# Performance work log

Hardware: AMD Instinct MI355X
Metric: run time of the kernel (lower is better)

The kernel has to match this reference:

```python
import jax, jax.numpy as jnp
import numpy as np

EMBED_DIM = 1024
NUM_HEADS = 16
HEAD_DIM = EMBED_DIM // NUM_HEADS


def setup_inputs() -> dict:
    key = jax.random.key(0)
    ks = jax.random.split(key, 9)
    B, L, D = 4, 2048, EMBED_DIM
    s = 1.0 / np.sqrt(D)
    return {
        "inputs": jax.random.normal(ks[0], (B, L, D), dtype=jnp.float32),
        "wq": jax.random.normal(ks[1], (D, D), dtype=jnp.float32) * s,
        "bq": jax.random.normal(ks[2], (D,), dtype=jnp.float32) * s,
        "wk": jax.random.normal(ks[3], (D, D), dtype=jnp.float32) * s,
        "bk": jax.random.normal(ks[4], (D,), dtype=jnp.float32) * s,
        "wv": jax.random.normal(ks[5], (D, D), dtype=jnp.float32) * s,
        "bv": jax.random.normal(ks[6], (D,), dtype=jnp.float32) * s,
        "wo": jax.random.normal(ks[7], (D, D), dtype=jnp.float32) * s,
        "bo": jax.random.normal(ks[8], (D,), dtype=jnp.float32) * s,
    }


def reference(inputs, wq, bq, wk, bk, wv, bv, wo, bo):
    B, L, D = inputs.shape
    H, Hd = NUM_HEADS, HEAD_DIM
    # Linear projections (torch Linear: x @ W^T + b)
    q = inputs @ wq.T + bq
    k = inputs @ wk.T + bk
    v = inputs @ wv.T + bv
    # (B, L, D) -> (B, H, L, Hd)
    q = q.reshape(B, L, H, Hd).transpose(0, 2, 1, 3)
    k = k.reshape(B, L, H, Hd).transpose(0, 2, 1, 3)
    v = v.reshape(B, L, H, Hd).transpose(0, 2, 1, 3)
    scale = 1.0 / np.sqrt(Hd).astype(np.float32)
    scores = jnp.einsum("bhqd,bhkd->bhqk", q, k) * scale  # (B,H,L,L)
    attn = jax.nn.softmax(scores, axis=-1)
    out = jnp.einsum("bhqk,bhkd->bhqd", attn, v)  # (B,H,L,Hd)
    out = out.transpose(0, 2, 1, 3).reshape(B, L, D)
    return out @ wo.T + bo
```

## Files before the change

kernel.cpp:

```cpp
#include <hip/hip_runtime.h>

typedef __attribute__((ext_vector_type(8))) short short8;
typedef __attribute__((ext_vector_type(8))) unsigned short ushort8;
typedef __attribute__((ext_vector_type(4))) unsigned short ushort4_t;
typedef __attribute__((ext_vector_type(4))) unsigned u32x4;
typedef __attribute__((ext_vector_type(4))) float f32x4;
typedef __attribute__((ext_vector_type(16))) float f32x16;

#define GLOAD_LDS(gp, lp) \
  __builtin_amdgcn_global_load_lds((const __attribute__((address_space(1))) void*)(gp), \
                                   (__attribute__((address_space(3))) void*)(lp), 16, 0, 0)

static __device__ __forceinline__ unsigned short f2bf(float f) {
  unsigned int u = __float_as_uint(f);
  u = u + 0x7fffu + ((u >> 16) & 1u);
  return (unsigned short)(u >> 16);
}

static __device__ __forceinline__ float exp2i(float x) {
  float r;
  asm("v_exp_f32 %0, %1" : "=v"(r) : "v"(x));
  return r;
}

static __device__ __forceinline__ unsigned cvtpk(float a, float b) {
  unsigned r;
  asm("v_cvt_pk_bf16_f32 %0, %1, %2" : "=v"(r) : "v"(a), "v"(b));
  return r;
}

static __device__ __forceinline__ void pl32swap(unsigned& a, unsigned& b) {
  asm("v_permlane32_swap_b32 %0, %1" : "+v"(a), "+v"(b));
}

__global__ __launch_bounds__(256) void cvt_all(const float* __restrict__ X,
                                               const float* __restrict__ w0, const float* __restrict__ w1,
                                               const float* __restrict__ w2, const float* __restrict__ w3,
                                               unsigned short* __restrict__ Xb,
                                               unsigned short* __restrict__ o0, unsigned short* __restrict__ o1,
                                               unsigned short* __restrict__ o2, unsigned short* __restrict__ o3) {
  int bid = blockIdx.x;
  const float* in;
  unsigned short* out;
  int i;
  if (bid < 4096) {
    in = X; out = Xb; i = bid * 2048 + threadIdx.x * 8;
  } else {
    int idx = bid - 4096;
    int w = idx >> 9;
    in = (w == 0) ? w0 : (w == 1) ? w1 : (w == 2) ? w2 : w3;
    out = (w == 0) ? o0 : (w == 1) ? o1 : (w == 2) ? o2 : o3;
    i = (idx & 511) * 2048 + threadIdx.x * 8;
  }
  const float4* p = reinterpret_cast<const float4*>(in + i);
  float4 a = p[0], b = p[1];
  ushort8 o;
  o[0] = f2bf(a.x); o[1] = f2bf(a.y); o[2] = f2bf(a.z); o[3] = f2bf(a.w);
  o[4] = f2bf(b.x); o[5] = f2bf(b.y); o[6] = f2bf(b.z); o[7] = f2bf(b.w);
  *reinterpret_cast<ushort8*>(out + i) = o;
}

template <int MODE, int BN>
__global__ __launch_bounds__(256) void gemm_bt(const unsigned short* __restrict__ A,
                                               const unsigned short* __restrict__ B,
                                               const float* __restrict__ bias,
                                               void* __restrict__ Cptr,
                                               int M, int N, int K, float scale) {
  constexpr int BCH = BN / 32;
  constexpr int NI = BN / 32;
  __shared__ char As[2][16384];
  __shared__ char Bs[2][BN * 128];
  const int t = threadIdx.x;
  const int lane = t & 63, wave = t >> 6;
  const int wm = wave >> 1, wn = wave & 1;
  const int m0 = blockIdx.y * 128, n0 = blockIdx.x * BN;

  const unsigned short* aS[4];
  const unsigned short* bS[BCH];
#pragma unroll
  for (int j = 0; j < 4; j++) {
    int i = wave * 256 + j * 64 + lane;
    int r = i >> 3, c = ((i & 7) ^ (r & 7)) << 3;
    aS[j] = A + (size_t)(m0 + r) * K + c;
  }
#pragma unroll
  for (int j = 0; j < BCH; j++) {
    int i = wave * (64 * BCH) + j * 64 + lane;
    int r = i >> 3, c = ((i & 7) ^ (r & 7)) << 3;
    bS[j] = B + (size_t)(n0 + r) * K + c;
  }

  f32x4 acc[4][NI] = {};
  const int NT = K >> 6;

#pragma unroll
  for (int j = 0; j < 4; j++) GLOAD_LDS(aS[j], As[0] + wave * 4096 + j * 1024);
#pragma unroll
  for (int j = 0; j < BCH; j++) GLOAD_LDS(bS[j], Bs[0] + wave * (1024 * BCH) + j * 1024);

  for (int kt = 0; kt < NT; kt++) {
    const int cur = kt & 1;
    __syncthreads();
    if (kt + 1 < NT) {
      int ko = (kt + 1) << 6;
#pragma unroll
      for (int j = 0; j < 4; j++) GLOAD_LDS(aS[j] + ko, As[cur ^ 1] + wave * 4096 + j * 1024);
#pragma unroll
      for (int j = 0; j < BCH; j++) GLOAD_LDS(bS[j] + ko, Bs[cur ^ 1] + wave * (1024 * BCH) + j * 1024);
    }
    const char* Ac = As[cur];
    const char* Bc = Bs[cur];
#pragma unroll
    for (int ks = 0; ks < 2; ks++) {
      short8 af[4], bfr[NI];
#pragma unroll
      for (int x = 0; x < 4; x++) {
        int arow = wm * 64 + x * 16 + (lane & 15);
        int kk = ks * 32 + (lane >> 4) * 8;
        af[x] = *reinterpret_cast<const short8*>(Ac + (((arow * 64 + kk) * 2) ^ ((arow & 7) << 4)));
      }
#pragma unroll
      for (int x = 0; x < NI; x++) {
        int brow = wn * (BN / 2) + x * 16 + (lane & 15);
        int kk = ks * 32 + (lane >> 4) * 8;
        bfr[x] = *reinterpret_cast<const short8*>(Bc + (((brow * 64 + kk) * 2) ^ ((brow & 7) << 4)));
      }
      __builtin_amdgcn_s_setprio(1);
#pragma unroll
      for (int mi = 0; mi < 4; mi++)
#pragma unroll
        for (int ni = 0; ni < NI; ni++)
          acc[mi][ni] = __builtin_amdgcn_mfma_f32_16x16x32_bf16(af[mi], bfr[ni], acc[mi][ni], 0, 0, 0);
      __builtin_amdgcn_s_setprio(0);
    }
  }

#pragma unroll
  for (int mi = 0; mi < 4; mi++) {
#pragma unroll
    for (int ni = 0; ni < NI; ni++) {
      int n = n0 + wn * (BN / 2) + ni * 16 + (lane & 15);
      float bs = bias[n];
      int mbase = m0 + wm * 64 + mi * 16 + ((lane >> 4) << 2);
      if (MODE == 2) {
        int b = mbase >> 11, l = mbase & 2047;
        ushort4_t o;
#pragma unroll
        for (int r = 0; r < 4; r++) o[r] = f2bf(acc[mi][ni][r] + bs);
        *reinterpret_cast<ushort4_t*>((unsigned short*)Cptr + (size_t)(b * N + n) * 2048 + l) = o;
      } else if (MODE == 0) {
#pragma unroll
        for (int r = 0; r < 4; r++)
          ((unsigned short*)Cptr)[(size_t)(mbase + r) * N + n] = f2bf((acc[mi][ni][r] + bs) * scale);
      } else {
#pragma unroll
        for (int r = 0; r < 4; r++)
          ((float*)Cptr)[(size_t)(mbase + r) * N + n] = acc[mi][ni][r] + bs;
      }
    }
  }
}

__global__ __launch_bounds__(256, 4) void attn_fwd(const unsigned short* __restrict__ Q,
                                                   const unsigned short* __restrict__ Kb,
                                                   const unsigned short* __restrict__ Vt,
                                                   unsigned short* __restrict__ O) {
  const int orig = blockIdx.x;
  const int wgid = (orig & 7) * 128 + (orig >> 3);
  const int qt = wgid & 15;
  const int h = (wgid >> 4) & 15;
  const int b = wgid >> 8;
  const int q0 = qt * 128;

  __shared__ char Ks[2][8192];
  __shared__ char Vs[2][8192];
  const int t = threadIdx.x, lane = t & 63, wave = t >> 6;
  const int ql = lane & 31;
  const int hi = lane >> 5;
  const int qrow = q0 + wave * 32 + ql;
  const int sw = (ql & 7) << 4;

  int lo_[4];
#pragma unroll
  for (int st = 0; st < 4; st++) lo_[st] = (ql * 128 + sw) ^ (st * 32 + hi * 16);

  const int ic0 = wave * 128 + lane, ic1 = ic0 + 64;
  const int r0 = ic0 >> 3, c0 = ((ic0 & 7) ^ (r0 & 7)) << 3;
  const int r1 = ic1 >> 3, c1 = ((ic1 & 7) ^ (r1 & 7)) << 3;
  const unsigned short* kS0 = Kb + (size_t)(b * 2048 + r0) * 1024 + h * 64 + c0;
  const unsigned short* kS1 = Kb + (size_t)(b * 2048 + r1) * 1024 + h * 64 + c1;
  const unsigned short* vS0 = Vt + ((size_t)(b * 16 + h) * 64 + r0) * 2048 + c0;
  const unsigned short* vS1 = Vt + ((size_t)(b * 16 + h) * 64 + r1) * 2048 + c1;

  short8 qf[4];
  {
    const unsigned short* qp = Q + (size_t)(b * 2048 + qrow) * 1024 + h * 64 + hi * 8;
#pragma unroll
    for (int st = 0; st < 4; st++) qf[st] = *reinterpret_cast<const short8*>(qp + st * 16);
  }

  const short one_bf = (short)0x3F80;
  const short8 ones = {one_bf, one_bf, one_bf, one_bf, one_bf, one_bf, one_bf, one_bf};

  f32x16 accd0 = {}, accd1 = {};
  f32x16 accl = {};

  GLOAD_LDS(kS0, Ks[0] + wave * 2048);
  GLOAD_LDS(kS1, Ks[0] + wave * 2048 + 1024);
  GLOAD_LDS(vS0, Vs[0] + wave * 2048);
  GLOAD_LDS(vS1, Vs[0] + wave * 2048 + 1024);

#pragma unroll 2
  for (int kt = 0; kt < 32; kt++) {
    const int cur = kt & 1;
    __syncthreads();
    if (kt + 1 < 32) {
      size_t ko = (size_t)(kt + 1) * 65536;
      int vo = (kt + 1) * 64;
      GLOAD_LDS(kS0 + ko, Ks[cur ^ 1] + wave * 2048);
      GLOAD_LDS(kS1 + ko, Ks[cur ^ 1] + wave * 2048 + 1024);
      GLOAD_LDS(vS0 + vo, Vs[cur ^ 1] + wave * 2048);
      GLOAD_LDS(vS1 + vo, Vs[cur ^ 1] + wave * 2048 + 1024);
    }
    const char* Kc = Ks[cur];
    const char* Vc = Vs[cur];

    f32x16 s0 = {}, s1 = {};
    __builtin_amdgcn_s_setprio(1);
#pragma unroll
    for (int st = 0; st < 4; st++) {
      short8 k0 = *reinterpret_cast<const short8*>(Kc + lo_[st]);
      short8 k1 = *reinterpret_cast<const short8*>(Kc + lo_[st] + 4096);
      s0 = __builtin_amdgcn_mfma_f32_32x32x16_bf16(k0, qf[st], s0, 0, 0, 0);
      s1 = __builtin_amdgcn_mfma_f32_32x32x16_bf16(k1, qf[st], s1, 0, 0, 0);
    }
    __builtin_amdgcn_s_setprio(0);

    short8 pf0, pf1, pf2, pf3;
    {
#pragma unroll
      for (int r = 0; r < 16; r++) s0[r] = exp2i(s0[r]);
      unsigned w0 = cvtpk(s0[0], s0[1]), w1 = cvtpk(s0[2], s0[3]);
      unsigned w2 = cvtpk(s0[4], s0[5]), w3 = cvtpk(s0[6], s0[7]);
      pl32swap(w0, w2); pl32swap(w1, w3);
      u32x4 p0 = {w0, w1, w2, w3};
      pf0 = __builtin_bit_cast(short8, p0);
      unsigned w4 = cvtpk(s0[8], s0[9]), w5 = cvtpk(s0[10], s0[11]);
      unsigned w6 = cvtpk(s0[12], s0[13]), w7 = cvtpk(s0[14], s0[15]);
      pl32swap(w4, w6); pl32swap(w5, w7);
      u32x4 p1 = {w4, w5, w6, w7};
      pf1 = __builtin_bit_cast(short8, p1);
    }
    {
#pragma unroll
      for (int r = 0; r < 16; r++) s1[r] = exp2i(s1[r]);
      unsigned x0 = cvtpk(s1[0], s1[1]), x1 = cvtpk(s1[2], s1[3]);
      unsigned x2 = cvtpk(s1[4], s1[5]), x3 = cvtpk(s1[6], s1[7]);
      pl32swap(x0, x2); pl32swap(x1, x3);
      u32x4 p2 = {x0, x1, x2, x3};
      pf2 = __builtin_bit_cast(short8, p2);
      unsigned x4 = cvtpk(s1[8], s1[9]), x5 = cvtpk(s1[10], s1[11]);
      unsigned x6 = cvtpk(s1[12], s1[13]), x7 = cvtpk(s1[14], s1[15]);
      pl32swap(x4, x6); pl32swap(x5, x7);
      u32x4 p3 = {x4, x5, x6, x7};
      pf3 = __builtin_bit_cast(short8, p3);
    }

    __builtin_amdgcn_s_setprio(1);
#pragma unroll
    for (int st = 0; st < 4; st++) {
      short8 pb = (st == 0) ? pf0 : (st == 1) ? pf1 : (st == 2) ? pf2 : pf3;
      short8 v0 = *reinterpret_cast<const short8*>(Vc + lo_[st]);
      short8 v1 = *reinterpret_cast<const short8*>(Vc + lo_[st] + 4096);
      accd0 = __builtin_amdgcn_mfma_f32_32x32x16_bf16(v0, pb, accd0, 0, 0, 0);
      accd1 = __builtin_amdgcn_mfma_f32_32x32x16_bf16(v1, pb, accd1, 0, 0, 0);
      accl  = __builtin_amdgcn_mfma_f32_32x32x16_bf16(ones, pb, accl, 0, 0, 0);
    }
    __builtin_amdgcn_s_setprio(0);
  }

  float inv = 1.0f / accl[0];
  unsigned short* op = O + (size_t)(b * 2048 + qrow) * 1024 + h * 64;
#pragma unroll
  for (int g = 0; g < 4; g++) {
    ushort4_t o0, o1;
#pragma unroll
    for (int j = 0; j < 4; j++) {
      o0[j] = f2bf(accd0[4 * g + j] * inv);
      o1[j] = f2bf(accd1[4 * g + j] * inv);
    }
    *reinterpret_cast<ushort4_t*>(op + 8 * g + 4 * hi) = o0;
    *reinterpret_cast<ushort4_t*>(op + 32 + 8 * g + 4 * hi) = o1;
  }
}

extern "C" void kernel_launch(void* const* d_in, const int* in_sizes, int n_in,
                              void* d_out, int out_size, void* d_ws, size_t ws_size,
                              hipStream_t stream) {
  const float* X = (const float*)d_in[0];
  const float* wq = (const float*)d_in[1];
  const float* bq = (const float*)d_in[2];
  const float* wk = (const float*)d_in[3];
  const float* bk = (const float*)d_in[4];
  const float* wv = (const float*)d_in[5];
  const float* bv = (const float*)d_in[6];
  const float* wo = (const float*)d_in[7];
  const float* bo = (const float*)d_in[8];

  char* ws = (char*)d_ws;
  const size_t MB = 1024 * 1024;
  unsigned short* Xb  = (unsigned short*)(ws + 0);
  unsigned short* Wqb = (unsigned short*)(ws + 16 * MB);
  unsigned short* Wkb = (unsigned short*)(ws + 18 * MB);
  unsigned short* Wvb = (unsigned short*)(ws + 20 * MB);
  unsigned short* Wob = (unsigned short*)(ws + 22 * MB);
  unsigned short* Qb  = (unsigned short*)(ws + 24 * MB);
  unsigned short* Kb  = (unsigned short*)(ws + 40 * MB);
  unsigned short* Vtb = (unsigned short*)(ws + 56 * MB);
  unsigned short* Ob  = (unsigned short*)(ws + 72 * MB);

  cvt_all<<<4096 + 4 * 512, 256, 0, stream>>>(X, wq, wk, wv, wo, Xb, Wqb, Wkb, Wvb, Wob);

  const float QSCALE = 0.125f * 1.4426950408889634f;
  gemm_bt<0, 128><<<dim3(8, 64), 256, 0, stream>>>(Xb, Wqb, bq, Qb, 8192, 1024, 1024, QSCALE);
  gemm_bt<0, 64><<<dim3(16, 64), 256, 0, stream>>>(Xb, Wkb, bk, Kb, 8192, 1024, 1024, 1.0f);
  gemm_bt<2, 128><<<dim3(8, 64), 256, 0, stream>>>(Xb, Wvb, bv, Vtb, 8192, 1024, 1024, 1.0f);

  attn_fwd<<<1024, 256, 0, stream>>>(Qb, Kb, Vtb, Ob);

  gemm_bt<1, 128><<<dim3(8, 64), 256, 0, stream>>>(Ob, Wob, bo, (float*)d_out, 8192, 1024, 1024, 1.0f);
}
```

Before: 206.0 us.

## Compute softmax denominator in registers and stage K/V through VGPRs

The attention kernel stops computing the row-sum with an extra MFMA against a ones vector each step. It instead sums the exponentials in registers and combines the two half-waves with a shuffle at the end, which removes a third of the PV-stage MFMAs. The async global-to-LDS prefetch is replaced by ordinary global loads into registers, written to LDS after the softmax, which changes how loads overlap with compute and adds register pressure and LDS stores. The K projection GEMM also switches to the 128-wide tile configuration.

```diff
diff --git a/kernel.cpp b/kernel.cpp
--- a/kernel.cpp
+++ b/kernel.cpp
@@ -199,11 +199,8 @@
     for (int st = 0; st < 4; st++) qf[st] = *reinterpret_cast<const short8*>(qp + st * 16);
   }
 
-  const short one_bf = (short)0x3F80;
-  const short8 ones = {one_bf, one_bf, one_bf, one_bf, one_bf, one_bf, one_bf, one_bf};
-
+  float l_run = 0.f;
   f32x16 accd0 = {}, accd1 = {};
-  f32x16 accl = {};
 
   GLOAD_LDS(kS0, Ks[0] + wave * 2048);
   GLOAD_LDS(kS1, Ks[0] + wave * 2048 + 1024);
@@ -214,13 +211,16 @@
   for (int kt = 0; kt < 32; kt++) {
     const int cur = kt & 1;
     __syncthreads();
-    if (kt + 1 < 32) {
-      size_t ko = (size_t)(kt + 1) * 65536;
-      int vo = (kt + 1) * 64;
-      GLOAD_LDS(kS0 + ko, Ks[cur ^ 1] + wave * 2048);
-      GLOAD_LDS(kS1 + ko, Ks[cur ^ 1] + wave * 2048 + 1024);
-      GLOAD_LDS(vS0 + vo, Vs[cur ^ 1] + wave * 2048);
-      GLOAD_LDS(vS1 + vo, Vs[cur ^ 1] + wave * 2048 + 1024);
+
+    const int ktn = (kt + 1) & 31;
+    short8 kr0, kr1, vr0, vr1;
+    {
+      size_t ko = (size_t)ktn * 65536;
+      int vo = ktn * 64;
+      kr0 = *reinterpret_cast<const short8*>(kS0 + ko);
+      kr1 = *reinterpret_cast<const short8*>(kS1 + ko);
+      vr0 = *reinterpret_cast<const short8*>(vS0 + vo);
+      vr1 = *reinterpret_cast<const short8*>(vS1 + vo);
     }
     const char* Kc = Ks[cur];
     const char* Vc = Vs[cur];
@@ -237,9 +237,15 @@
     __builtin_amdgcn_s_setprio(0);
 
     short8 pf0, pf1, pf2, pf3;
+    float rs;
     {
 #pragma unroll
       for (int r = 0; r < 16; r++) s0[r] = exp2i(s0[r]);
+      float a0 = (s0[0] + s0[1]) + (s0[2] + s0[3]);
+      float a1 = (s0[4] + s0[5]) + (s0[6] + s0[7]);
+      float a2 = (s0[8] + s0[9]) + (s0[10] + s0[11]);
+      float a3 = (s0[12] + s0[13]) + (s0[14] + s0[15]);
+      rs = (a0 + a1) + (a2 + a3);
       unsigned w0 = cvtpk(s0[0], s0[1]), w1 = cvtpk(s0[2], s0[3]);
       unsigned w2 = cvtpk(s0[4], s0[5]), w3 = cvtpk(s0[6], s0[7]);
       pl32swap(w0, w2); pl32swap(w1, w3);
@@ -254,6 +260,11 @@
     {
 #pragma unroll
       for (int r = 0; r < 16; r++) s1[r] = exp2i(s1[r]);
+      float a0 = (s1[0] + s1[1]) + (s1[2] + s1[3]);
+      float a1 = (s1[4] + s1[5]) + (s1[6] + s1[7]);
+      float a2 = (s1[8] + s1[9]) + (s1[10] + s1[11]);
+      float a3 = (s1[12] + s1[13]) + (s1[14] + s1[15]);
+      rs += (a0 + a1) + (a2 + a3);
       unsigned x0 = cvtpk(s1[0], s1[1]), x1 = cvtpk(s1[2], s1[3]);
       unsigned x2 = cvtpk(s1[4], s1[5]), x3 = cvtpk(s1[6], s1[7]);
       pl32swap(x0, x2); pl32swap(x1, x3);
@@ -265,6 +276,16 @@
       u32x4 p3 = {x4, x5, x6, x7};
       pf3 = __builtin_bit_cast(short8, p3);
     }
+    l_run += rs;
+
+    if (kt < 31) {
+      char* kd = Ks[cur ^ 1] + wave * 2048 + (lane << 4);
+      *reinterpret_cast<short8*>(kd) = kr0;
+      *reinterpret_cast<short8*>(kd + 1024) = kr1;
+      char* vd = Vs[cur ^ 1] + wave * 2048 + (lane << 4);
+      *reinterpret_cast<short8*>(vd) = vr0;
+      *reinterpret_cast<short8*>(vd + 1024) = vr1;
+    }
 
     __builtin_amdgcn_s_setprio(1);
 #pragma unroll
@@ -274,12 +295,12 @@
       short8 v1 = *reinterpret_cast<const short8*>(Vc + lo_[st] + 4096);
       accd0 = __builtin_amdgcn_mfma_f32_32x32x16_bf16(v0, pb, accd0, 0, 0, 0);
       accd1 = __builtin_amdgcn_mfma_f32_32x32x16_bf16(v1, pb, accd1, 0, 0, 0);
-      accl  = __builtin_amdgcn_mfma_f32_32x32x16_bf16(ones, pb, accl, 0, 0, 0);
     }
     __builtin_amdgcn_s_setprio(0);
   }
 
-  float inv = 1.0f / accl[0];
+  float l_tot = l_run + __shfl_xor(l_run, 32);
+  float inv = 1.0f / l_tot;
   unsigned short* op = O + (size_t)(b * 2048 + qrow) * 1024 + h * 64;
 #pragma unroll
   for (int g = 0; g < 4; g++) {
@@ -323,7 +344,7 @@
 
   const float QSCALE = 0.125f * 1.4426950408889634f;
   gemm_bt<0, 128><<<dim3(8, 64), 256, 0, stream>>>(Xb, Wqb, bq, Qb, 8192, 1024, 1024, QSCALE);
-  gemm_bt<0, 64><<<dim3(16, 64), 256, 0, stream>>>(Xb, Wkb, bk, Kb, 8192, 1024, 1024, 1.0f);
+  gemm_bt<0, 128><<<dim3(8, 64), 256, 0, stream>>>(Xb, Wkb, bk, Kb, 8192, 1024, 1024, 1.0f);
   gemm_bt<2, 128><<<dim3(8, 64), 256, 0, stream>>>(Xb, Wvb, bv, Vtb, 8192, 1024, 1024, 1.0f);
 
   attn_fwd<<<1024, 256, 0, stream>>>(Qb, Kb, Vtb, Ob);
```

New measurement: 378.4 us. 1.84x slower.
